# Kernel tuning notes

Measured on AMD Instinct MI355X. Metric: run time of the kernel, lower is better.

## Reference

```python
import jax, jax.numpy as jnp
import numpy as np

B, D, OUT = 8192, 1024, 256
H1, H2 = 8, 4
EPS = 1e-5


def setup_inputs() -> dict:
    key = jax.random.key(0)
    ks = jax.random.split(key, 8)
    sc = lambda k, shape: jax.random.normal(k, shape, jnp.float32) * 0.05
    return {
        "x": jax.random.normal(ks[0], (B, D), jnp.float32),
        "W1": sc(ks[1], (D, H1, 1)),      # D diagonal blocks of the masked Linear(D -> 8D)
        "b1": sc(ks[2], (D * H1,)),
        "g1": jnp.ones((D * H1,), jnp.float32),
        "be1": jnp.zeros((D * H1,), jnp.float32),
        "W2": sc(ks[3], (D, H2, H1)),     # D diagonal blocks of the masked Linear(8D -> 4D)
        "b2": sc(ks[4], (D * H2,)),
        "g2": jnp.ones((D * H2,), jnp.float32),
        "be2": jnp.zeros((D * H2,), jnp.float32),
        "Wfc": sc(ks[5], (OUT, D * H2)),
        "bfc": sc(ks[6], (OUT,)),
    }


def _batchnorm(h, g, b):
    # BatchNorm1d in training mode: per-channel batch mean, biased variance
    mu = h.mean(axis=0)
    var = h.var(axis=0)  # ddof=0 (biased), matching torch normalization
    return g * (h - mu) * jax.lax.rsqrt(var + EPS) + b


def reference(x, W1, b1, g1, be1, W2, b2, g2, be2, Wfc, bfc):
    n = x.shape[0]
    # layer 1: per-feature (1 -> H1) block GEMM == masked dense Linear
    h = jnp.einsum("bdi,doi->bdo", x[:, :, None], W1).reshape(n, D * H1)
    h = jax.nn.relu(_batchnorm(h + b1, g1, be1))
    # layer 2: per-feature (H1 -> H2) block GEMM
    h = jnp.einsum("bdi,doi->bdo", h.reshape(n, D, H1), W2).reshape(n, D * H2)
    h = jax.nn.relu(_batchnorm(h + b2, g2, be2))
    # dense output head
    return h @ Wfc.T + bfc
```

## Files before the change

### kernel.cpp

```cpp
#include <hip/hip_runtime.h>

#define EPSV 1e-5f

typedef short bf16x8 __attribute__((ext_vector_type(8)));
typedef float f32x4 __attribute__((ext_vector_type(4)));
typedef const __attribute__((address_space(1))) unsigned int gu32;
typedef __attribute__((address_space(3))) unsigned int lu32;

static __device__ __forceinline__ unsigned short f2b(float f) {
  union { float f; unsigned u; } v; v.f = f;
  return (unsigned short)((v.u + 0x7fffu + ((v.u >> 16) & 1u)) >> 16);
}

__global__ void k_pre(const float* __restrict__ wfc, unsigned short* __restrict__ wb,
                      const float* __restrict__ x, float* __restrict__ ps1) {
  if (blockIdx.x < 512) {
    const int f = blockIdx.x * 256 + threadIdx.x;
    const int l15 = f & 15, quad = (f >> 4) & 3, nb = (f >> 6) & 15, k32b = f >> 10;
    const int n = nb * 16 + l15;
    const int k = k32b * 32 + quad * 8;
    const float4* src = (const float4*)(wfc + (size_t)n * 4096 + k);
    float4 a = src[0], b = src[1];
    ushort4 o0, o1;
    o0.x = f2b(a.x); o0.y = f2b(a.y); o0.z = f2b(a.z); o0.w = f2b(a.w);
    o1.x = f2b(b.x); o1.y = f2b(b.y); o1.z = f2b(b.z); o1.w = f2b(b.w);
    *(ushort4*)(wb + (size_t)f * 8) = o0;
    *(ushort4*)(wb + (size_t)f * 8 + 4) = o1;
  } else {
    const int blk = blockIdx.x - 512;
    const int c = threadIdx.x * 4;
    const int r0 = blk * 32;
    float4 s = {0.f,0.f,0.f,0.f}, q = {0.f,0.f,0.f,0.f};
    for (int g = 0; g < 4; ++g) {
      float4 v[8];
#pragma unroll
      for (int j = 0; j < 8; ++j)
        v[j] = *(const float4*)(x + (size_t)(r0 + g*8 + j) * 1024 + c);
#pragma unroll
      for (int j = 0; j < 8; ++j) {
        s.x += v[j].x; s.y += v[j].y; s.z += v[j].z; s.w += v[j].w;
        q.x = fmaf(v[j].x, v[j].x, q.x); q.y = fmaf(v[j].y, v[j].y, q.y);
        q.z = fmaf(v[j].z, v[j].z, q.z); q.w = fmaf(v[j].w, v[j].w, q.w);
      }
    }
    *(float4*)(ps1 + (size_t)blk * 2048 + c) = s;
    *(float4*)(ps1 + (size_t)blk * 2048 + 1024 + c) = q;
  }
}

__global__ __launch_bounds__(256) void k_fin1(const float* __restrict__ ps1,
    const float* __restrict__ W1, const float* __restrict__ g1,
    const float* __restrict__ be1, float* __restrict__ pt) {
  __shared__ float redS[8][32], redQ[8][32];
  const int t = threadIdx.x;
  const int d0 = blockIdx.x * 32;
  const int dl = t & 31, slot = t >> 5;
  float s = 0.f, q = 0.f;
  for (int u = 0; u < 32; u += 8) {
#pragma unroll
    for (int w = 0; w < 8; ++w) {
      const size_t base = (size_t)(slot * 32 + u + w) * 2048 + d0 + dl;
      s += ps1[base];
      q += ps1[base + 1024];
    }
  }
  redS[slot][dl] = s; redQ[slot][dl] = q;
  __syncthreads();
  const int dloc = t >> 3, i = t & 7;
  float xs = 0.f, xq = 0.f;
#pragma unroll
  for (int p = 0; p < 8; ++p) { xs += redS[p][dloc]; xq += redQ[p][dloc]; }
  const float inv = 1.f / 8192.f;
  const int d = d0 + dloc;
  const int c = d * 8 + i;
  float mean = xs * inv;
  float var = xq * inv - mean * mean;
  float w = W1[c];
  float s1 = g1[c] * w * rsqrtf(w * w * var + EPSV);
  float t1 = be1[c] - s1 * mean;
  pt[(size_t)d * 52 + i] = s1;
  pt[(size_t)d * 52 + 8 + i] = t1;
}

__global__ __launch_bounds__(256) void k_stats2(const float* __restrict__ x,
    const float* __restrict__ pt, const float* __restrict__ W2,
    float* __restrict__ ps2s, float* __restrict__ ps2q) {
  __shared__ float red[8][32][8];
  const int t = threadIdx.x;
  const int dl = t & 31, slot = t >> 5;
  const int d = blockIdx.x * 32 + dl;
  float s1v[8], t1v[8], w2v[32];
  {
    const f32x4* pq = (const f32x4*)(pt + (size_t)d * 52);
    f32x4 a = pq[0], b = pq[1], c = pq[2], e = pq[3];
#pragma unroll
    for (int j = 0; j < 4; ++j) {
      s1v[j] = a[j]; s1v[4 + j] = b[j];
      t1v[j] = c[j]; t1v[4 + j] = e[j];
    }
  }
  const float4* wp = (const float4*)(W2 + (size_t)d * 32);
#pragma unroll
  for (int i = 0; i < 8; ++i) {
    float4 v = wp[i];
    w2v[i*4+0]=v.x; w2v[i*4+1]=v.y; w2v[i*4+2]=v.z; w2v[i*4+3]=v.w;
  }
  float s[4] = {0.f,0.f,0.f,0.f}, q[4] = {0.f,0.f,0.f,0.f};
  const int b0 = blockIdx.y * 256 + slot * 32;
  for (int r = 0; r < 32; r += 8) {
    float xv[8];
#pragma unroll
    for (int j = 0; j < 8; ++j)
      xv[j] = x[(size_t)(b0 + r + j) * 1024 + d];
#pragma unroll
    for (int j = 0; j < 8; ++j) {
      float a1[8];
#pragma unroll
      for (int i = 0; i < 8; ++i) a1[i] = fmaxf(fmaf(s1v[i], xv[j], t1v[i]), 0.f);
#pragma unroll
      for (int o = 0; o < 4; ++o) {
        float h = 0.f;
#pragma unroll
        for (int i = 0; i < 8; ++i) h = fmaf(a1[i], w2v[o*8+i], h);
        s[o] += h;
        q[o] = fmaf(h, h, q[o]);
      }
    }
  }
#pragma unroll
  for (int j = 0; j < 4; ++j) {
    red[slot][dl][j] = s[j];
    red[slot][dl][4+j] = q[j];
  }
  __syncthreads();
  const int d2l = t >> 3, j = t & 7;
  float v = 0.f;
#pragma unroll
  for (int p = 0; p < 8; ++p) v += red[p][d2l][j];
  const int c2 = (blockIdx.x * 32 + d2l) * 4 + (t & 3);
  if (j < 4) ps2s[(size_t)blockIdx.y * 4096 + c2] = v;
  else       ps2q[(size_t)blockIdx.y * 4096 + c2] = v;
}

__global__ void k_fin2(const float* __restrict__ W2, const float* __restrict__ g2,
                       const float* __restrict__ be2, const float* __restrict__ ps2s,
                       const float* __restrict__ ps2q, float* __restrict__ pt) {
  const int c2 = blockIdx.x * 256 + threadIdx.x;
  const int d = c2 >> 2, o = c2 & 3;
  float sm = 0.f, sq = 0.f;
#pragma unroll
  for (int b = 0; b < 32; ++b) {
    sm += ps2s[(size_t)b * 4096 + c2];
    sq += ps2q[(size_t)b * 4096 + c2];
  }
  const float inv = 1.f / 8192.f;
  float m = sm * inv;
  float var = sq * inv - m * m;
  float s2 = g2[c2] * rsqrtf(var + EPSV);
  float t2 = be2[c2] - s2 * m;
  pt[(size_t)d * 52 + 48 + o] = t2;
#pragma unroll
  for (int i = 0; i < 8; ++i)
    pt[(size_t)d * 52 + 16 + o * 8 + i] = W2[(size_t)d * 32 + o * 8 + i] * s2;
}

__global__ __launch_bounds__(512, 4) void k_gemm(const float* __restrict__ x,
    const float* __restrict__ pt, const unsigned short* __restrict__ wb,
    const float* __restrict__ bfc, float* __restrict__ out,
    float* __restrict__ part, const int use_part) {
  __shared__ __align__(16) unsigned short Bs[2][32 * 512];
  __shared__ __align__(16) unsigned short As[64 * 72];
  __shared__ __align__(16) float Ps[16 * 52];
  const int t = threadIdx.x;
  const int lane = t & 63;
  const int wv = t >> 6;
  const int wM = wv >> 2;
  const int wN = wv & 3;
  const int m0 = blockIdx.x * 64;
  const int kQ = blockIdx.y;
  const int quad = lane >> 4;
  const int l15 = lane & 15;
  const int dloc = t & 15, rowg = t >> 4;
  const int d0 = kQ * 128;
  const int k32q = kQ * 16;

  f32x4 acc[2][4];
#pragma unroll
  for (int mt = 0; mt < 2; ++mt)
#pragma unroll
    for (int nt = 0; nt < 4; ++nt) {
      f32x4 z = {0.f, 0.f, 0.f, 0.f};
      acc[mt][nt] = z;
    }

  float xv[2];

#define STAGE_B(CH, BUF) do {                                               \
    const int k32b0_ = k32q + (CH) * 2;                                     \
    _Pragma("unroll")                                                       \
    for (int j_ = 0; j_ < 4; ++j_) {                                        \
      const int fl_ = j_ * 8 + wv;                                          \
      const int gfrag_ = (k32b0_ + (fl_ >> 4)) * 16 + (fl_ & 15);           \
      const unsigned short* gp_ = wb + ((size_t)gfrag_ * 64 + lane) * 8;    \
      __builtin_amdgcn_global_load_lds((gu32*)gp_,                          \
          (lu32*)&Bs[BUF][fl_ * 512], 16, 0, 0);                            \
    }                                                                       \
  } while (0)

#define STAGE_P(CH) do {                                                    \
    if (t < 208) {                                                          \
      const float* gp_ = pt + (size_t)(d0 + (CH) * 16) * 52 + t * 4;        \
      __builtin_amdgcn_global_load_lds((gu32*)gp_,                          \
          (lu32*)&Ps[t * 4], 16, 0, 0);                                     \
    }                                                                       \
  } while (0)

#define PRE_X(CH) do {                                                      \
    const int d_ = d0 + (CH) * 16 + dloc;                                   \
    _Pragma("unroll")                                                       \
    for (int r_ = 0; r_ < 2; ++r_)                                          \
      xv[r_] = x[(size_t)(m0 + rowg * 2 + r_) * 1024 + d_];                 \
  } while (0)

#define GEN_A() do {                                                        \
    const f32x4* pq_ = (const f32x4*)&Ps[dloc * 52];                        \
    float pv_[52];                                                          \
    _Pragma("unroll")                                                       \
    for (int i_ = 0; i_ < 13; ++i_) {                                       \
      f32x4 v_ = pq_[i_];                                                   \
      pv_[i_*4+0] = v_[0]; pv_[i_*4+1] = v_[1];                             \
      pv_[i_*4+2] = v_[2]; pv_[i_*4+3] = v_[3];                             \
    }                                                                       \
    _Pragma("unroll")                                                       \
    for (int r_ = 0; r_ < 2; ++r_) {                                        \
      const float xvv_ = xv[r_];                                            \
      float a1_[8];                                                         \
      _Pragma("unroll")                                                     \
      for (int i_ = 0; i_ < 8; ++i_)                                        \
        a1_[i_] = fmaxf(fmaf(pv_[i_], xvv_, pv_[8 + i_]), 0.f);             \
      unsigned short o4_[4];                                                \
      _Pragma("unroll")                                                     \
      for (int o_ = 0; o_ < 4; ++o_) {                                      \
        float h_ = pv_[48 + o_];                                            \
        _Pragma("unroll")                                                   \
        for (int i_ = 0; i_ < 8; ++i_)                                      \
          h_ = fmaf(a1_[i_], pv_[16 + o_ * 8 + i_], h_);                    \
        o4_[o_] = f2b(fmaxf(h_, 0.f));                                      \
      }                                                                     \
      *(ushort4*)&As[(rowg * 2 + r_) * 72 + dloc * 4] =                     \
          make_ushort4(o4_[0], o4_[1], o4_[2], o4_[3]);                     \
    }                                                                       \
  } while (0)

  STAGE_P(0);
  STAGE_B(0, 0);
  PRE_X(0);
  __syncthreads();
  GEN_A();
  __syncthreads();

  for (int chi = 0; chi < 8; ++chi) {
    const int cur = chi & 1;
    if (chi < 7) {
      PRE_X(chi + 1);
      STAGE_P(chi + 1);
    }
#pragma unroll
    for (int kk = 0; kk < 2; ++kk) {
      bf16x8 af[2];
#pragma unroll
      for (int mt = 0; mt < 2; ++mt)
        af[mt] = *(const bf16x8*)&As[(wM * 32 + mt * 16 + l15) * 72 + kk * 32 + quad * 8];
#pragma unroll
      for (int nt = 0; nt < 4; ++nt) {
        const int fl = kk * 16 + wN * 4 + nt;
        bf16x8 bfr = *(const bf16x8*)&Bs[cur][fl * 512 + lane * 8];
#pragma unroll
        for (int mt = 0; mt < 2; ++mt)
          acc[mt][nt] = __builtin_amdgcn_mfma_f32_16x16x32_bf16(af[mt], bfr,
                                                                acc[mt][nt], 0, 0, 0);
      }
    }
    __syncthreads();
    if (chi < 7) {
      STAGE_B(chi + 1, cur ^ 1);
      GEN_A();
    }
    __syncthreads();
  }

#undef STAGE_B
#undef STAGE_P
#undef PRE_X
#undef GEN_A

  if (use_part) {
    float* dst = part + (size_t)kQ * (8192 * 256);
#pragma unroll
    for (int nt = 0; nt < 4; ++nt) {
      const int col = wN * 64 + nt * 16 + l15;
#pragma unroll
      for (int mt = 0; mt < 2; ++mt) {
#pragma unroll
        for (int r = 0; r < 4; ++r) {
          const int row = m0 + wM * 32 + mt * 16 + quad * 4 + r;
          dst[(size_t)row * 256 + col] = acc[mt][nt][r];
        }
      }
    }
  } else {
#pragma unroll
    for (int nt = 0; nt < 4; ++nt) {
      const int col = wN * 64 + nt * 16 + l15;
      const float bias = (kQ == 0) ? bfc[col] : 0.f;
#pragma unroll
      for (int mt = 0; mt < 2; ++mt) {
#pragma unroll
        for (int r = 0; r < 4; ++r) {
          const int row = m0 + wM * 32 + mt * 16 + quad * 4 + r;
          atomicAdd(&out[(size_t)row * 256 + col], acc[mt][nt][r] + bias);
        }
      }
    }
  }
}

__global__ void k_merge(const float* __restrict__ part, const float* __restrict__ bfc,
                        float* __restrict__ out) {
  const size_t i = (size_t)blockIdx.x * 256 + threadIdx.x;
  const size_t SL = (size_t)8192 * 256;
  f32x4 s = ((const f32x4*)part)[i];
#pragma unroll
  for (int k = 1; k < 8; ++k)
    s += ((const f32x4*)(part + (size_t)k * SL))[i];
  const int col = (int)((i * 4) & 255);
  s += *(const f32x4*)(bfc + col);
  ((f32x4*)out)[i] = s;
}

extern "C" void kernel_launch(void* const* d_in, const int* in_sizes, int n_in,
                              void* d_out, int out_size, void* d_ws, size_t ws_size,
                              hipStream_t stream) {
  const float* x   = (const float*)d_in[0];
  const float* W1  = (const float*)d_in[1];
  const float* g1  = (const float*)d_in[3];
  const float* be1 = (const float*)d_in[4];
  const float* W2  = (const float*)d_in[5];
  const float* g2  = (const float*)d_in[7];
  const float* be2 = (const float*)d_in[8];
  const float* Wfc = (const float*)d_in[9];
  const float* bfc = (const float*)d_in[10];
  float* out = (float*)d_out;

  char* ws = (char*)d_ws;
  unsigned short* wb = (unsigned short*)ws;
  float* pt     = (float*)(ws + (2u << 20));
  float* shared = (float*)(ws + (2u << 20) + (256u << 10));
  float* ps1  = shared;
  float* ps2s = shared;
  float* ps2q = shared + 32 * 4096;

  const size_t PART_OFF = (2u << 20) + (256u << 10) + (2u << 20);
  const size_t PART_SZ  = (size_t)8 * 8192 * 256 * sizeof(float);
  float* part = (float*)(ws + PART_OFF);
  const int use_part = (ws_size >= PART_OFF + PART_SZ) ? 1 : 0;

  if (!use_part)
    hipMemsetAsync(d_out, 0, (size_t)out_size * sizeof(float), stream);

  k_pre   <<<dim3(768),    256, 0, stream>>>(Wfc, wb, x, ps1);
  k_fin1  <<<dim3(32),     256, 0, stream>>>(ps1, W1, g1, be1, pt);
  k_stats2<<<dim3(32, 32), 256, 0, stream>>>(x, pt, W2, ps2s, ps2q);
  k_fin2  <<<dim3(16),     256, 0, stream>>>(W2, g2, be2, ps2s, ps2q, pt);
  k_gemm  <<<dim3(128, 8), 512, 0, stream>>>(x, pt, wb, bfc, out, part, use_part);
  if (use_part)
    k_merge<<<dim3(2048),  256, 0, stream>>>(part, bfc, out);
}
```

Baseline: 167.3 us.

## Double k-chunk per iteration in fused GEMM and pack A-generation math into float2

Each iteration of the fused GEMM loop now covers 32 features (128 K values) instead of 16. This halves the number of loop iterations and barrier pairs and doubles the size of the B, A and parameter LDS tiles. Each thread now builds four A rows, processed in pairs with two-wide vector FMA helpers so the compiler can emit packed fp32 instructions. The larger LDS footprint forces launch_bounds down from 4 to 2 blocks per CU, trading occupancy and latency hiding for fewer synchronisations and more work per stage.

```diff
diff --git a/kernel.cpp b/kernel.cpp
--- a/kernel.cpp
+++ b/kernel.cpp
@@ -4,12 +4,20 @@
 
 typedef short bf16x8 __attribute__((ext_vector_type(8)));
 typedef float f32x4 __attribute__((ext_vector_type(4)));
+typedef float f32x2 __attribute__((ext_vector_type(2)));
 typedef const __attribute__((address_space(1))) unsigned int gu32;
 typedef __attribute__((address_space(3))) unsigned int lu32;
 
 static __device__ __forceinline__ unsigned short f2b(float f) {
   union { float f; unsigned u; } v; v.f = f;
   return (unsigned short)((v.u + 0x7fffu + ((v.u >> 16) & 1u)) >> 16);
+}
+
+static __device__ __forceinline__ f32x2 pk_fma(f32x2 a, f32x2 b, f32x2 c) {
+  f32x2 r; r[0] = fmaf(a[0], b[0], c[0]); r[1] = fmaf(a[1], b[1], c[1]); return r;
+}
+static __device__ __forceinline__ f32x2 pk_max0(f32x2 a) {
+  f32x2 r; r[0] = fmaxf(a[0], 0.f); r[1] = fmaxf(a[1], 0.f); return r;
 }
 
 __global__ void k_pre(const float* __restrict__ wfc, unsigned short* __restrict__ wb,
@@ -164,13 +172,13 @@
     pt[(size_t)d * 52 + 16 + o * 8 + i] = W2[(size_t)d * 32 + o * 8 + i] * s2;
 }
 
-__global__ __launch_bounds__(512, 4) void k_gemm(const float* __restrict__ x,
+__global__ __launch_bounds__(512, 2) void k_gemm(const float* __restrict__ x,
     const float* __restrict__ pt, const unsigned short* __restrict__ wb,
     const float* __restrict__ bfc, float* __restrict__ out,
     float* __restrict__ part, const int use_part) {
-  __shared__ __align__(16) unsigned short Bs[2][32 * 512];
-  __shared__ __align__(16) unsigned short As[64 * 72];
-  __shared__ __align__(16) float Ps[16 * 52];
+  __shared__ __align__(16) unsigned short Bs[2][64 * 512];
+  __shared__ __align__(16) unsigned short As[64 * 136];
+  __shared__ __align__(16) float Ps[32 * 52];
   const int t = threadIdx.x;
   const int lane = t & 63;
   const int wv = t >> 6;
@@ -180,7 +188,7 @@
   const int kQ = blockIdx.y;
   const int quad = lane >> 4;
   const int l15 = lane & 15;
-  const int dloc = t & 15, rowg = t >> 4;
+  const int dloc = t & 31, rowg = t >> 5;
   const int d0 = kQ * 128;
   const int k32q = kQ * 16;
 
@@ -193,12 +201,12 @@
       acc[mt][nt] = z;
     }
 
-  float xv[2];
+  float xv[4];
 
 #define STAGE_B(CH, BUF) do {                                               \
-    const int k32b0_ = k32q + (CH) * 2;                                     \
+    const int k32b0_ = k32q + (CH) * 4;                                     \
     _Pragma("unroll")                                                       \
-    for (int j_ = 0; j_ < 4; ++j_) {                                        \
+    for (int j_ = 0; j_ < 8; ++j_) {                                        \
       const int fl_ = j_ * 8 + wv;                                          \
       const int gfrag_ = (k32b0_ + (fl_ >> 4)) * 16 + (fl_ & 15);           \
       const unsigned short* gp_ = wb + ((size_t)gfrag_ * 64 + lane) * 8;    \
@@ -208,18 +216,18 @@
   } while (0)
 
 #define STAGE_P(CH) do {                                                    \
-    if (t < 208) {                                                          \
-      const float* gp_ = pt + (size_t)(d0 + (CH) * 16) * 52 + t * 4;        \
+    if (t < 416) {                                                          \
+      const float* gp_ = pt + (size_t)(d0 + (CH) * 32) * 52 + t * 4;        \
       __builtin_amdgcn_global_load_lds((gu32*)gp_,                          \
           (lu32*)&Ps[t * 4], 16, 0, 0);                                     \
     }                                                                       \
   } while (0)
 
 #define PRE_X(CH) do {                                                      \
-    const int d_ = d0 + (CH) * 16 + dloc;                                   \
+    const int d_ = d0 + (CH) * 32 + dloc;                                   \
     _Pragma("unroll")                                                       \
-    for (int r_ = 0; r_ < 2; ++r_)                                          \
-      xv[r_] = x[(size_t)(m0 + rowg * 2 + r_) * 1024 + d_];                 \
+    for (int r_ = 0; r_ < 4; ++r_)                                          \
+      xv[r_] = x[(size_t)(m0 + rowg * 4 + r_) * 1024 + d_];                 \
   } while (0)
 
 #define GEN_A() do {                                                        \
@@ -232,23 +240,34 @@
       pv_[i_*4+2] = v_[2]; pv_[i_*4+3] = v_[3];                             \
     }                                                                       \
     _Pragma("unroll")                                                       \
-    for (int r_ = 0; r_ < 2; ++r_) {                                        \
-      const float xvv_ = xv[r_];                                            \
-      float a1_[8];                                                         \
+    for (int pr_ = 0; pr_ < 2; ++pr_) {                                     \
+      f32x2 xp_; xp_[0] = xv[pr_*2]; xp_[1] = xv[pr_*2+1];                  \
+      f32x2 a1_[8];                                                         \
       _Pragma("unroll")                                                     \
-      for (int i_ = 0; i_ < 8; ++i_)                                        \
-        a1_[i_] = fmaxf(fmaf(pv_[i_], xvv_, pv_[8 + i_]), 0.f);             \
-      unsigned short o4_[4];                                                \
+      for (int i_ = 0; i_ < 8; ++i_) {                                      \
+        f32x2 b_; b_[0] = pv_[i_];    b_[1] = pv_[i_];                      \
+        f32x2 c_; c_[0] = pv_[8+i_];  c_[1] = pv_[8+i_];                    \
+        a1_[i_] = pk_max0(pk_fma(b_, xp_, c_));                             \
+      }                                                                     \
+      f32x2 h_[4];                                                          \
       _Pragma("unroll")                                                     \
       for (int o_ = 0; o_ < 4; ++o_) {                                      \
-        float h_ = pv_[48 + o_];                                            \
+        h_[o_][0] = pv_[48 + o_]; h_[o_][1] = pv_[48 + o_];                 \
         _Pragma("unroll")                                                   \
-        for (int i_ = 0; i_ < 8; ++i_)                                      \
-          h_ = fmaf(a1_[i_], pv_[16 + o_ * 8 + i_], h_);                    \
-        o4_[o_] = f2b(fmaxf(h_, 0.f));                                      \
+        for (int i_ = 0; i_ < 8; ++i_) {                                    \
+          f32x2 w_; w_[0] = pv_[16 + o_*8 + i_]; w_[1] = w_[0];             \
+          h_[o_] = pk_fma(a1_[i_], w_, h_[o_]);                             \
+        }                                                                   \
       }                                                                     \
-      *(ushort4*)&As[(rowg * 2 + r_) * 72 + dloc * 4] =                     \
-          make_ushort4(o4_[0], o4_[1], o4_[2], o4_[3]);                     \
+      _Pragma("unroll")                                                     \
+      for (int rr_ = 0; rr_ < 2; ++rr_) {                                   \
+        unsigned short o4_[4];                                              \
+        _Pragma("unroll")                                                   \
+        for (int o_ = 0; o_ < 4; ++o_)                                      \
+          o4_[o_] = f2b(fmaxf(h_[o_][rr_], 0.f));                           \
+        *(ushort4*)&As[(rowg * 4 + pr_ * 2 + rr_) * 136 + dloc * 4] =       \
+            make_ushort4(o4_[0], o4_[1], o4_[2], o4_[3]);                   \
+      }                                                                     \
     }                                                                       \
   } while (0)
 
@@ -259,18 +278,18 @@
   GEN_A();
   __syncthreads();
 
-  for (int chi = 0; chi < 8; ++chi) {
+  for (int chi = 0; chi < 4; ++chi) {
     const int cur = chi & 1;
-    if (chi < 7) {
+    if (chi < 3) {
       PRE_X(chi + 1);
       STAGE_P(chi + 1);
     }
 #pragma unroll
-    for (int kk = 0; kk < 2; ++kk) {
+    for (int kk = 0; kk < 4; ++kk) {
       bf16x8 af[2];
 #pragma unroll
       for (int mt = 0; mt < 2; ++mt)
-        af[mt] = *(const bf16x8*)&As[(wM * 32 + mt * 16 + l15) * 72 + kk * 32 + quad * 8];
+        af[mt] = *(const bf16x8*)&As[(wM * 32 + mt * 16 + l15) * 136 + kk * 32 + quad * 8];
 #pragma unroll
       for (int nt = 0; nt < 4; ++nt) {
         const int fl = kk * 16 + wN * 4 + nt;
@@ -282,7 +301,7 @@
       }
     }
     __syncthreads();
-    if (chi < 7) {
+    if (chi < 3) {
       STAGE_B(chi + 1, cur ^ 1);
       GEN_A();
     }
```

New measurement: 174.7 us. 4.4% more time.
